# Kernel optimization log

Measured on AMD Instinct MI355X. Metric: run time of the kernel, lower is better.

The kernel has to match this reference:

```python
import jax, jax.numpy as jnp
import numpy as np

LN_EPS = 1e-5

def setup_inputs() -> dict:
    key = jax.random.key(0)
    ks = jax.random.split(key, 4)
    B, N, D, De = 4, 2048, 128, 8
    h = jax.random.normal(ks[0], (B, N, D), dtype=jnp.float32)
    e = jax.random.normal(ks[1], (B, N, N, De), dtype=jnp.float32)
    W_w = jax.random.normal(ks[2], (D, D), dtype=jnp.float32) * (1.0 / np.sqrt(D))
    W_b = jax.random.normal(ks[3], (D,), dtype=jnp.float32) * 0.02
    ln_g = jnp.ones((D,), dtype=jnp.float32)
    ln_b = jnp.zeros((D,), dtype=jnp.float32)
    return {"h": h, "e": e, "W_w": W_w, "W_b": W_b, "ln_g": ln_g, "ln_b": ln_b}

def _layernorm(x, g, b):
    mu = jnp.mean(x, axis=-1, keepdims=True)
    var = jnp.var(x, axis=-1, keepdims=True)
    return (x - mu) * jax.lax.rsqrt(var + LN_EPS) * g + b

def reference(h, e, W_w, W_b, ln_g, ln_b):
    # w_ij = softmax_j(||e_ij||)  -> [B, N, N]
    scores = jnp.linalg.norm(e, axis=-1)          # [B, N, N]
    w = jax.nn.softmax(scores, axis=2)            # softmax over neighbor dim j
    # agg_i = sum_j w_ij * h_j  (batched matmul instead of O(B N^2 D) broadcast)
    agg = jnp.einsum('bij,bjd->bid', w, h)        # [B, N, D]
    z = (h + agg) @ W_w.T + W_b                   # Linear
    h_new = jax.nn.relu(_layernorm(z, ln_g, ln_b)) + h
    return (h_new, e)
```

## Files before the change

### kernel.cpp

```cpp
#include <hip/hip_runtime.h>
#include <hip/hip_bf16.h>
#include <math.h>

constexpr int B  = 4;
constexpr int N  = 2048;
constexpr int D  = 128;
constexpr int De = 8;
constexpr int KS = 8;
constexpr float LN_EPS = 1e-5f;

typedef __bf16 bf16x8 __attribute__((ext_vector_type(8)));
typedef float  f32x4v __attribute__((ext_vector_type(4)));

__device__ inline ushort f2bf(float f) {
    uint u = __float_as_uint(f);
    return (ushort)((u + 0x7fffu + ((u >> 16) & 1u)) >> 16);
}

__global__ __launch_bounds__(256) void k_escore(const float* __restrict__ e,
                                                float* __restrict__ out_e,
                                                uint* __restrict__ w16) {
    long long tid = (long long)blockIdx.x * 256 + threadIdx.x;
    const float4* src = reinterpret_cast<const float4*>(e + tid * 2 * De);
    float4 a0 = src[0];
    float4 a1 = src[1];
    float4 a2 = src[2];
    float4 a3 = src[3];
    float4* dst = reinterpret_cast<float4*>(out_e + tid * 2 * De);
    dst[0] = a0; dst[1] = a1; dst[2] = a2; dst[3] = a3;
    float s0 = a0.x*a0.x + a0.y*a0.y + a0.z*a0.z + a0.w*a0.w
             + a1.x*a1.x + a1.y*a1.y + a1.z*a1.z + a1.w*a1.w;
    float s1 = a2.x*a2.x + a2.y*a2.y + a2.z*a2.z + a2.w*a2.w
             + a3.x*a3.x + a3.y*a3.y + a3.z*a3.z + a3.w*a3.w;
    uint p0 = f2bf(__expf(sqrtf(s0)));
    uint p1 = f2bf(__expf(sqrtf(s1)));
    w16[tid] = p0 | (p1 << 16);
}

__global__ __launch_bounds__(256) void k_hcast(const float* __restrict__ h,
                                               ushort* __restrict__ hT16) {
    __shared__ float tile[32][33];
    int b  = blockIdx.z;
    int n0 = blockIdx.x * 32, d0 = blockIdx.y * 32;
    int t  = threadIdx.x;
    int r = t >> 3, c = (t & 7) * 4;
    float4 v = *reinterpret_cast<const float4*>(h + ((long long)b * N + n0 + r) * D + d0 + c);
    tile[r][c] = v.x; tile[r][c + 1] = v.y; tile[r][c + 2] = v.z; tile[r][c + 3] = v.w;
    __syncthreads();
    ushort4 o;
    o.x = f2bf(tile[c + 0][r]);
    o.y = f2bf(tile[c + 1][r]);
    o.z = f2bf(tile[c + 2][r]);
    o.w = f2bf(tile[c + 3][r]);
    *reinterpret_cast<ushort4*>(hT16 + ((long long)b * D + d0 + r) * N + n0 + c) = o;
}

__global__ __launch_bounds__(256) void k_rowsum(const ushort* __restrict__ w16,
                                                float* __restrict__ inv_rowsum) {
    __shared__ float red[4];
    long long row = blockIdx.x;
    int t = threadIdx.x;
    uint4 v = *reinterpret_cast<const uint4*>(w16 + row * (long long)N + t * 8);
    uint u[4] = {v.x, v.y, v.z, v.w};
    float s = 0.0f;
    #pragma unroll
    for (int q = 0; q < 4; ++q) {
        s += __uint_as_float(u[q] << 16);
        s += __uint_as_float(u[q] & 0xffff0000u);
    }
    #pragma unroll
    for (int off = 32; off > 0; off >>= 1) s += __shfl_xor(s, off);
    if ((t & 63) == 0) red[t >> 6] = s;
    __syncthreads();
    if (t == 0)
        inv_rowsum[row] = 1.0f / (red[0] + red[1] + red[2] + red[3]);
}

__global__ __launch_bounds__(256) void k_agg(const ushort* __restrict__ w16,
                                             const ushort* __restrict__ hT16,
                                             float* __restrict__ aggp) {
    constexpr int BM = 64;
    constexpr int BK = 32;
    constexpr int KC = N / KS;
    __shared__ ushort A_s[BM][40];
    __shared__ ushort B_s[D][40];

    int b  = blockIdx.y;
    int i0 = blockIdx.x * BM;
    int kbase = blockIdx.z * KC;
    int t  = threadIdx.x;
    int wid = t >> 6, lane = t & 63;
    int wr = wid >> 1, wc = wid & 1;
    int lr = lane & 15, lk = (lane >> 4) * 8;

    const ushort* wb = w16 + ((long long)b * N + i0) * N + kbase;
    const ushort* hb = hT16 + (long long)b * D * N + kbase;

    f32x4v acc[2][4] = {};

    int ar = t >> 2, ac = (t & 3) * 8;
    int q1 = t + 256;

    for (int k0 = 0; k0 < KC; k0 += BK) {
        uint4 av  = *reinterpret_cast<const uint4*>(wb + (long long)ar * N + k0 + ac);
        uint4 bv0 = *reinterpret_cast<const uint4*>(hb + (long long)(t >> 2) * N + k0 + (t & 3) * 8);
        uint4 bv1 = *reinterpret_cast<const uint4*>(hb + (long long)(q1 >> 2) * N + k0 + (q1 & 3) * 8);

        __syncthreads();

        *reinterpret_cast<uint4*>(&A_s[ar][ac]) = av;
        *reinterpret_cast<uint4*>(&B_s[t >> 2][(t & 3) * 8]) = bv0;
        *reinterpret_cast<uint4*>(&B_s[q1 >> 2][(q1 & 3) * 8]) = bv1;

        __syncthreads();

        bf16x8 af[2], bfr[4];
        #pragma unroll
        for (int fm = 0; fm < 2; ++fm)
            af[fm] = *reinterpret_cast<const bf16x8*>(&A_s[wr * 32 + fm * 16 + lr][lk]);
        #pragma unroll
        for (int fn = 0; fn < 4; ++fn)
            bfr[fn] = *reinterpret_cast<const bf16x8*>(&B_s[wc * 64 + fn * 16 + lr][lk]);
        #pragma unroll
        for (int fm = 0; fm < 2; ++fm)
            #pragma unroll
            for (int fn = 0; fn < 4; ++fn)
                acc[fm][fn] = __builtin_amdgcn_mfma_f32_16x16x32_bf16(
                    af[fm], bfr[fn], acc[fm][fn], 0, 0, 0);
    }

    float* ap = aggp + (long long)blockIdx.z * B * N * D + ((long long)b * N + i0) * D;
    #pragma unroll
    for (int fm = 0; fm < 2; ++fm)
        #pragma unroll
        for (int fn = 0; fn < 4; ++fn)
            #pragma unroll
            for (int r = 0; r < 4; ++r) {
                int row = wr * 32 + fm * 16 + (lane >> 4) * 4 + r;
                int col = wc * 64 + fn * 16 + lr;
                ap[(long long)row * D + col] = acc[fm][fn][r];
            }
}

__global__ __launch_bounds__(128) void k_out(const float* __restrict__ h,
                                             const float* __restrict__ aggp,
                                             const float* __restrict__ inv_rowsum,
                                             const float* __restrict__ Ww,
                                             const float* __restrict__ Wb,
                                             const float* __restrict__ ln_g,
                                             const float* __restrict__ ln_b,
                                             float* __restrict__ out) {
    __shared__ __align__(16) float x_s[D];
    __shared__ float red[4];
    constexpr long long BND = (long long)B * N * D;

    long long row = blockIdx.x;
    int d = threadIdx.x;

    float hv = h[row * D + d];
    float a = 0.0f;
    #pragma unroll
    for (int s = 0; s < KS; ++s)
        a += aggp[s * BND + row * D + d];
    a *= inv_rowsum[row];
    x_s[d] = hv + a;
    __syncthreads();

    const float4* wrow = reinterpret_cast<const float4*>(Ww + (long long)d * D);
    const float4* xv   = reinterpret_cast<const float4*>(x_s);
    float z = 0.0f;
    #pragma unroll
    for (int k = 0; k < D / 4; ++k) {
        float4 wv = wrow[k];
        float4 vv = xv[k];
        z += wv.x * vv.x + wv.y * vv.y + wv.z * vv.z + wv.w * vv.w;
    }
    z += Wb[d];

    float s = z;
    #pragma unroll
    for (int off = 32; off > 0; off >>= 1) s += __shfl_xor(s, off);
    if ((d & 63) == 0) red[d >> 6] = s;
    __syncthreads();
    float mu = (red[0] + red[1]) * (1.0f / (float)D);
    __syncthreads();

    float dev = z - mu;
    float s2 = dev * dev;
    #pragma unroll
    for (int off = 32; off > 0; off >>= 1) s2 += __shfl_xor(s2, off);
    if ((d & 63) == 0) red[d >> 6] = s2;
    __syncthreads();
    float var = (red[0] + red[1]) * (1.0f / (float)D);

    float y = dev * rsqrtf(var + LN_EPS) * ln_g[d] + ln_b[d];
    out[row * D + d] = fmaxf(y, 0.0f) + hv;
}

extern "C" void kernel_launch(void* const* d_in, const int* in_sizes, int n_in,
                              void* d_out, int out_size, void* d_ws, size_t ws_size,
                              hipStream_t stream) {
    const float* h    = (const float*)d_in[0];
    const float* e    = (const float*)d_in[1];
    const float* Ww   = (const float*)d_in[2];
    const float* Wb   = (const float*)d_in[3];
    const float* ln_g = (const float*)d_in[4];
    const float* ln_b = (const float*)d_in[5];

    float* out   = (float*)d_out;
    float* out_h = out;
    float* out_e = out + (size_t)B * N * D;

    ushort* w16  = (ushort*)d_ws;
    ushort* hT16 = w16 + (size_t)B * N * N;
    float*  aggp = (float*)(hT16 + (size_t)B * D * N);
    float*  inv_rowsum = aggp + (size_t)KS * B * N * D;

    long long threads = (long long)B * N * N / 2;

    k_escore<<<(int)(threads / 256), 256, 0, stream>>>(e, out_e, (uint*)w16);
    dim3 gh(N / 32, D / 32, B);
    k_hcast<<<gh, 256, 0, stream>>>(h, hT16);
    k_rowsum<<<B * N, 256, 0, stream>>>(w16, inv_rowsum);
    dim3 g2(N / 64, B, KS);
    k_agg<<<g2, 256, 0, stream>>>(w16, hT16, aggp);
    k_out<<<B * N, 128, 0, stream>>>(h, aggp, inv_rowsum, Ww, Wb, ln_g, ln_b, out_h);
}
```

Before: 329.1 us.

## Coalesce edge-score loads across lanes and prefetch next GEMM tile into registers

The edge-score kernel now has each lane read one contiguous float4, so a wavefront covers consecutive memory instead of each thread striding over 64 bytes. Partial squared norms are combined with lane shuffles, and every fourth lane writes the packed pair of bf16 weights. Separately, the aggregation GEMM loads the next K-tile of global data into registers right after the shared-memory store, so that load overlaps the MFMA work. The shuffle-based pairing adds some cross-lane traffic and leaves three of four lanes idle on the store, and the register prefetch raises register pressure.

```diff
diff --git a/kernel.cpp b/kernel.cpp
--- a/kernel.cpp
+++ b/kernel.cpp
@@ -19,22 +19,25 @@
 
 __global__ __launch_bounds__(256) void k_escore(const float* __restrict__ e,
                                                 float* __restrict__ out_e,
-                                                uint* __restrict__ w16) {
-    long long tid = (long long)blockIdx.x * 256 + threadIdx.x;
-    const float4* src = reinterpret_cast<const float4*>(e + tid * 2 * De);
-    float4 a0 = src[0];
-    float4 a1 = src[1];
-    float4 a2 = src[2];
-    float4 a3 = src[3];
-    float4* dst = reinterpret_cast<float4*>(out_e + tid * 2 * De);
-    dst[0] = a0; dst[1] = a1; dst[2] = a2; dst[3] = a3;
-    float s0 = a0.x*a0.x + a0.y*a0.y + a0.z*a0.z + a0.w*a0.w
-             + a1.x*a1.x + a1.y*a1.y + a1.z*a1.z + a1.w*a1.w;
-    float s1 = a2.x*a2.x + a2.y*a2.y + a2.z*a2.z + a2.w*a2.w
-             + a3.x*a3.x + a3.y*a3.y + a3.z*a3.z + a3.w*a3.w;
-    uint p0 = f2bf(__expf(sqrtf(s0)));
-    uint p1 = f2bf(__expf(sqrtf(s1)));
-    w16[tid] = p0 | (p1 << 16);
+                                                uint* __restrict__ w32) {
+    const float4* src = reinterpret_cast<const float4*>(e);
+    float4*       dst = reinterpret_cast<float4*>(out_e);
+    long long base = (long long)blockIdx.x * 1024;
+    int t = threadIdx.x;
+
+    #pragma unroll
+    for (int p = 0; p < 4; ++p) {
+        long long i4 = base + p * 256 + t;
+        float4 v = src[i4];
+        dst[i4] = v;
+        float ss = v.x * v.x + v.y * v.y + v.z * v.z + v.w * v.w;
+        ss += __shfl_xor(ss, 1);
+        float val = __expf(sqrtf(ss));
+        uint bf = f2bf(val);
+        uint partner = (uint)__shfl_xor((int)bf, 2);
+        if ((t & 3) == 0)
+            w32[i4 >> 2] = bf | (partner << 16);
+    }
 }
 
 __global__ __launch_bounds__(256) void k_hcast(const float* __restrict__ h,
@@ -101,18 +104,23 @@
     int ar = t >> 2, ac = (t & 3) * 8;
     int q1 = t + 256;
 
+    uint4 av  = *reinterpret_cast<const uint4*>(wb + (long long)ar * N + ac);
+    uint4 bv0 = *reinterpret_cast<const uint4*>(hb + (long long)(t >> 2) * N + (t & 3) * 8);
+    uint4 bv1 = *reinterpret_cast<const uint4*>(hb + (long long)(q1 >> 2) * N + (q1 & 3) * 8);
+
     for (int k0 = 0; k0 < KC; k0 += BK) {
-        uint4 av  = *reinterpret_cast<const uint4*>(wb + (long long)ar * N + k0 + ac);
-        uint4 bv0 = *reinterpret_cast<const uint4*>(hb + (long long)(t >> 2) * N + k0 + (t & 3) * 8);
-        uint4 bv1 = *reinterpret_cast<const uint4*>(hb + (long long)(q1 >> 2) * N + k0 + (q1 & 3) * 8);
-
         __syncthreads();
-
         *reinterpret_cast<uint4*>(&A_s[ar][ac]) = av;
         *reinterpret_cast<uint4*>(&B_s[t >> 2][(t & 3) * 8]) = bv0;
         *reinterpret_cast<uint4*>(&B_s[q1 >> 2][(q1 & 3) * 8]) = bv1;
-
         __syncthreads();
+
+        int kn = k0 + BK;
+        if (kn < KC) {
+            av  = *reinterpret_cast<const uint4*>(wb + (long long)ar * N + kn + ac);
+            bv0 = *reinterpret_cast<const uint4*>(hb + (long long)(t >> 2) * N + kn + (t & 3) * 8);
+            bv1 = *reinterpret_cast<const uint4*>(hb + (long long)(q1 >> 2) * N + kn + (q1 & 3) * 8);
+        }
 
         bf16x8 af[2], bfr[4];
         #pragma unroll
@@ -216,12 +224,13 @@
     float*  aggp = (float*)(hT16 + (size_t)B * D * N);
     float*  inv_rowsum = aggp + (size_t)KS * B * N * D;
 
-    long long threads = (long long)B * N * N / 2;
-
-    k_escore<<<(int)(threads / 256), 256, 0, stream>>>(e, out_e, (uint*)w16);
+    long long total_f4 = (long long)B * N * N * De / 4;
+    int eblocks = (int)(total_f4 / 1024);
+
+    k_escore<<<eblocks, 256, 0, stream>>>(e, out_e, (uint*)w16);
     dim3 gh(N / 32, D / 32, B);
     k_hcast<<<gh, 256, 0, stream>>>(h, hT16);
-    k_rowsum<<<B * N, 256, 0, stream>>>(w16, inv_rowsum);
+    k_rowsum<<<B * N, 256, 0, stream>>>(w16, (float*)inv_rowsum);
     dim3 g2(N / 64, B, KS);
     k_agg<<<g2, 256, 0, stream>>>(w16, hT16, aggp);
     k_out<<<B * N, 128, 0, stream>>>(h, aggp, inv_rowsum, Ww, Wb, ln_g, ln_b, out_h);
```

Result: faster. 290.1 us (-11.8%).
